# Kernel optimization log

Measured on AMD Instinct MI355X. Metric: run time of the kernel, lower is better.

The kernel has to match this reference:

```python
import jax, jax.numpy as jnp
import numpy as np

B, S, D, H, DFF = 8, 1024, 1024, 16, 4096
DK = D // H
NEG = -1000000000.0


def layernorm(x, g, b, eps=1e-5):
    mu = jnp.mean(x, axis=-1, keepdims=True)
    var = jnp.mean((x - mu) ** 2, axis=-1, keepdims=True)
    return (x - mu) / jnp.sqrt(var + eps) * g + b


def setup_inputs() -> dict:
    key = jax.random.key(0)
    ks = jax.random.split(key, 16)
    s = 0.02
    inp = {
        "x": jax.random.normal(ks[0], (B, S, D), jnp.float32),
        "binary_mask": jax.random.randint(ks[1], (B, S), 0, 2, jnp.int32),
        # per-head projections stacked: [H, D, DK]
        "Wq": jax.random.normal(ks[2], (H, D, DK), jnp.float32) * s,
        "bq": jnp.zeros((H, DK), jnp.float32),
        "Wk": jax.random.normal(ks[3], (H, D, DK), jnp.float32) * s,
        "bk": jnp.zeros((H, DK), jnp.float32),
        "Wv": jax.random.normal(ks[4], (H, D, DK), jnp.float32) * s,
        "bv": jnp.zeros((H, DK), jnp.float32),
        "Wo": jax.random.normal(ks[5], (D, D), jnp.float32) * s,
        "bo": jnp.zeros((D,), jnp.float32),
        "ga": jnp.ones((D,), jnp.float32),
        "ba": jnp.zeros((D,), jnp.float32),
        "W1": jax.random.normal(ks[6], (D, DFF), jnp.float32) * s,
        "b1": jnp.zeros((DFF,), jnp.float32),
        "W2": jax.random.normal(ks[7], (DFF, D), jnp.float32) * s,
        "b2": jnp.zeros((D,), jnp.float32),
        "gf": jnp.ones((D,), jnp.float32),
        "bf": jnp.zeros((D,), jnp.float32),
    }
    return inp


def encoder_fwd(x, binary_mask, Wq, bq, Wk, bk, Wv, bv, Wo, bo, ga, ba, W1, b1, W2, b2, gf, bf):
    # --- multi-head self-attention (heads vectorized over h axis) ---
    q = jnp.einsum("bsd,hdk->bhsk", x, Wq) + bq[None, :, None, :]
    k = jnp.einsum("bsd,hdk->bhsk", x, Wk) + bk[None, :, None, :]
    v = jnp.einsum("bsd,hdk->bhsk", x, Wv) + bv[None, :, None, :]
    score = jnp.einsum("bhik,bhjk->bhij", q, k) / jnp.sqrt(jnp.float32(DK))
    # mask: binary_mask is over KEY positions, broadcast over query dim
    score = score + jnp.where(binary_mask[:, None, None, :] == 0, NEG, 0.0)
    # NOTE: original code softmaxes over dim=1 of [B,Sq,Sk] -> the QUERY axis
    probs = jax.nn.softmax(score, axis=2)
    ctx = jnp.einsum("bhij,bhjk->bhik", probs, v)  # [B,H,S,DK]
    ctx = jnp.transpose(ctx, (0, 2, 1, 3)).reshape(x.shape[0], x.shape[1], D)
    attn_out = ctx @ Wo + bo
    y = layernorm(x + attn_out, ga, ba)
    # --- FFN ---
    h = jax.nn.relu(y @ W1 + b1)
    ffn_out = h @ W2 + b2
    return layernorm(y + ffn_out, gf, bf)


def reference(x, binary_mask, Wq, bq, Wk, bk, Wv, bv, Wo, bo, ga, ba, W1, b1, W2, b2, gf, bf):
    return encoder_fwd(x, binary_mask, Wq, bq, Wk, bk, Wv, bv, Wo, bo, ga, ba, W1, b1, W2, b2, gf, bf)
```

## Files before the change

### kernel.cpp

```cpp
#include <hip/hip_runtime.h>
#include <hip/hip_bf16.h>

typedef __bf16 bf16;
typedef __bf16 bf16x8 __attribute__((ext_vector_type(8)));
typedef __bf16 bf16x4 __attribute__((ext_vector_type(4)));
typedef float  f32x4  __attribute__((ext_vector_type(4)));

#define NB 8
#define NS 1024
#define ND 1024
#define NH 16
#define NDK 64
#define NDFF 4096

static __device__ __forceinline__ f32x4 mfma16(bf16x8 a, bf16x8 b, f32x4 c) {
    return __builtin_amdgcn_mfma_f32_16x16x32_bf16(a, b, c, 0, 0, 0);
}

#define GLDS(g, l) __builtin_amdgcn_global_load_lds( \
    (const __attribute__((address_space(1))) void*)(g), \
    (__attribute__((address_space(3))) void*)(l), 16, 0, 0)

__global__ __launch_bounds__(256) void cvt_x(const float* __restrict__ in,
                                             bf16* __restrict__ out, int n4)
{
    int idx = blockIdx.x * 256 + threadIdx.x;
    if (idx >= n4) return;
    float4 v = ((const float4*)in)[idx];
    bf16x4 o = { (bf16)v.x, (bf16)v.y, (bf16)v.z, (bf16)v.w };
    ((bf16x4*)out)[idx] = o;
}

__global__ __launch_bounds__(256) void prep_transpose(
    const float* __restrict__ Wq, const float* __restrict__ Wk, const float* __restrict__ Wv,
    const float* __restrict__ Wo, const float* __restrict__ W1, const float* __restrict__ W2,
    bf16* __restrict__ wqkvT, bf16* __restrict__ WoT,
    bf16* __restrict__ W1T, bf16* __restrict__ W2T)
{
    __shared__ float T[64][65];
    int bid = blockIdx.x;
    const float* src; bf16* dst; int srcLd, dstLd, tR, tC; bool scale = false;
    if (bid < 768) {
        int mat = bid >> 4, ty = bid & 15;
        int h = mat & 15, type = mat >> 4;
        const float* W = (type == 0) ? Wq : (type == 1 ? Wk : Wv);
        src = W + (size_t)h * ND * NDK;
        srcLd = NDK; tR = ty * 64; tC = 0;
        dst = wqkvT + ((size_t)type * 1024 + h * 64) * ND;
        dstLd = ND;
        scale = (type == 0);
    } else if (bid < 1024) {
        int b2 = bid - 768; int ty = b2 >> 4, tx = b2 & 15;
        src = Wo; srcLd = ND; tR = ty * 64; tC = tx * 64; dst = WoT; dstLd = ND;
    } else if (bid < 2048) {
        int b2 = bid - 1024; int ty = b2 >> 6, tx = b2 & 63;
        src = W1; srcLd = NDFF; tR = ty * 64; tC = tx * 64; dst = W1T; dstLd = ND;
    } else {
        int b2 = bid - 2048; int ty = b2 >> 4, tx = b2 & 15;
        src = W2; srcLd = ND; tR = ty * 64; tC = tx * 64; dst = W2T; dstLd = NDFF;
    }
    int t = threadIdx.x;
    int c0 = t & 63, r0 = t >> 6;
    #pragma unroll
    for (int rr = 0; rr < 16; rr++) {
        int row = rr * 4 + r0;
        T[row][c0] = src[(size_t)(tR + row) * srcLd + tC + c0];
    }
    __syncthreads();
    #pragma unroll
    for (int cc = 0; cc < 16; cc++) {
        int col = cc * 4 + r0;
        float v = T[c0][col];
        if (scale) v *= 0.125f;
        dst[(size_t)(tC + col) * dstLd + tR + c0] = (bf16)v;
    }
}

__global__ void prep_bias(const float* __restrict__ bq, const float* __restrict__ bk,
                          const float* __restrict__ bv, float* __restrict__ bqkv)
{
    int n = blockIdx.x * 256 + threadIdx.x;
    if (n >= 3072) return;
    int type = n >> 10, hk = n & 1023;
    const float* bb = (type == 0) ? bq : (type == 1 ? bk : bv);
    float v = bb[hk];
    if (type == 0) v *= 0.125f;
    bqkv[n] = v;
}

template<int BN>
__device__ __forceinline__ void gemm256_core(
    const bf16* __restrict__ A, const bf16* __restrict__ BT, int K,
    int rowBase, int colBase, f32x4 (&acc)[8][BN / 64],
    bf16* As, bf16* Bs)
{
    constexpr int NJ = BN / 128;
    constexpr int ABUF = 256 * 64;
    constexpr int BBUF = BN * 64;
    const int tid = threadIdx.x;
    const int lane = tid & 63, wid = tid >> 6;
    const int wm = wid >> 2, wn = wid & 3;
    const int lrow = lane & 15, lq = lane >> 4;
    const int srow = lane >> 3, gblk = (lane & 7) ^ srow;
    const int co0 = (lq ^ (lrow & 7)) * 8;
    const int co1 = ((4 + lq) ^ (lrow & 7)) * 8;

    f32x4 zz = {0.f, 0.f, 0.f, 0.f};
    #pragma unroll
    for (int i = 0; i < 8; i++)
        #pragma unroll
        for (int j = 0; j < 2 * NJ; j++) acc[i][j] = zz;

    const bf16* Ag = A  + (size_t)(rowBase + wid * 8 + srow) * K + gblk * 8;
    const bf16* Bg = BT + (size_t)(colBase + wid * 8 + srow) * K + gblk * 8;

#define STAGE256(kt, bi) do { \
    const bf16* a_ = Ag + (size_t)(kt) * 64; \
    _Pragma("unroll") \
    for (int r_ = 0; r_ < 4; r_++) \
        GLDS(a_ + (size_t)r_ * 64 * K, As + (bi) * ABUF + (r_ * 64 + wid * 8) * 64); \
    const bf16* b_ = Bg + (size_t)(kt) * 64; \
    _Pragma("unroll") \
    for (int r_ = 0; r_ < BN / 64; r_++) \
        GLDS(b_ + (size_t)r_ * 64 * K, Bs + (bi) * BBUF + (r_ * 64 + wid * 8) * 64); \
} while (0)

#define READ_A(MS) \
    _Pragma("unroll") \
    for (int i_ = 0; i_ < 4; i_++) { \
        int ro_ = (wm * 128 + (MS) * 64 + i_ * 16 + lrow) * 64; \
        af[i_][0] = *(const bf16x8*)&Ab[ro_ + co0]; \
        af[i_][1] = *(const bf16x8*)&Ab[ro_ + co1]; \
    }

#define READ_B(NS_) \
    _Pragma("unroll") \
    for (int j_ = 0; j_ < NJ; j_++) { \
        int ro_ = (wn * (BN / 4) + (NS_) * (BN / 8) + j_ * 16 + lrow) * 64; \
        bfr[j_][0] = *(const bf16x8*)&Bb[ro_ + co0]; \
        bfr[j_][1] = *(const bf16x8*)&Bb[ro_ + co1]; \
    }

#define MFMA_CLUSTER(IOFF, JOFF) do { \
    __builtin_amdgcn_s_barrier(); \
    asm volatile("s_waitcnt lgkmcnt(0)" ::: "memory"); \
    __builtin_amdgcn_sched_barrier(0); \
    __builtin_amdgcn_s_setprio(1); \
    _Pragma("unroll") \
    for (int i_ = 0; i_ < 4; i_++) \
        _Pragma("unroll") \
        for (int j_ = 0; j_ < NJ; j_++) { \
            acc[(IOFF) + i_][(JOFF) + j_] = mfma16(af[i_][0], bfr[j_][0], acc[(IOFF) + i_][(JOFF) + j_]); \
            acc[(IOFF) + i_][(JOFF) + j_] = mfma16(af[i_][1], bfr[j_][1], acc[(IOFF) + i_][(JOFF) + j_]); \
        } \
    __builtin_amdgcn_s_setprio(0); \
} while (0)

    const int nt = K >> 6;
    STAGE256(0, 0);
    asm volatile("s_waitcnt vmcnt(0)" ::: "memory");
    __builtin_amdgcn_s_barrier();

    int cur = 0;
    for (int t = 0; t < nt; ++t, cur ^= 1) {
        const bf16* Ab = As + cur * ABUF;
        const bf16* Bb = Bs + cur * BBUF;
        bf16x8 af[4][2], bfr[NJ][2];
        READ_A(0); READ_B(0);
        if (t + 1 < nt) STAGE256(t + 1, cur ^ 1);
        MFMA_CLUSTER(0, 0);
        __builtin_amdgcn_s_barrier();
        READ_A(1);
        MFMA_CLUSTER(4, 0);
        __builtin_amdgcn_s_barrier();
        READ_B(1);
        MFMA_CLUSTER(4, NJ);
        __builtin_amdgcn_s_barrier();
        READ_A(0);
        MFMA_CLUSTER(0, NJ);
        asm volatile("s_waitcnt vmcnt(0)" ::: "memory");
        __builtin_amdgcn_s_barrier();
    }
#undef STAGE256
#undef READ_A
#undef READ_B
#undef MFMA_CLUSTER
}

__global__ __launch_bounds__(512, 2) void g1_qkv(
    const bf16* __restrict__ x, const bf16* __restrict__ wqkvT, const float* __restrict__ bqkv,
    bf16* __restrict__ Q, bf16* __restrict__ Kb, bf16* __restrict__ Vb)
{
    __shared__ bf16 As[2 * 256 * 64], Bs[2 * 128 * 64];
    f32x4 acc[8][2];
    int nwg = gridDim.x, g = blockIdx.x;
    int sw = (g & 7) * (nwg >> 3) + (g >> 3);
    int bm = sw / 24, bn = sw % 24;
    int rowBase = bm * 256, colBase = bn * 128;
    gemm256_core<128>(x, wqkvT, ND, rowBase, colBase, acc, As, Bs);
    const int tid = threadIdx.x, lane = tid & 63, wid = tid >> 6;
    const int wm = wid >> 2, wn = wid & 3, lrow = lane & 15, lq = lane >> 4;
    #pragma unroll
    for (int j = 0; j < 2; j++) {
        int gcol = colBase + wn * 32 + j * 16 + lrow;
        float bias = bqkv[gcol];
        int type = gcol >> 10, h = (gcol >> 6) & 15, kk = gcol & 63;
        bf16* dst = (type == 0) ? Q : (type == 1 ? Kb : Vb);
        #pragma unroll
        for (int i = 0; i < 8; i++) {
            #pragma unroll
            for (int r = 0; r < 4; r++) {
                int grow = rowBase + wm * 128 + i * 16 + lq * 4 + r;
                int b = grow >> 10, s = grow & 1023;
                dst[((size_t)(b * NH + h) * NS + s) * NDK + kk] = (bf16)(acc[i][j][r] + bias);
            }
        }
    }
}

__global__ __launch_bounds__(256) void vt_trans(
    const bf16* __restrict__ Vb, bf16* __restrict__ Vt)
{
    __shared__ bf16 T[64 * 72];
    int bh = blockIdx.y, s0 = blockIdx.x * 64;
    const bf16* src = Vb + ((size_t)bh * NS + s0) * NDK;
    int tid = threadIdx.x;
    #pragma unroll
    for (int it = 0; it < 2; it++) {
        int g = tid + it * 256;
        int row = g >> 3, c = (g & 7) * 8;
        *(bf16x8*)&T[row * 72 + c] = *(const bf16x8*)&src[row * NDK + c];
    }
    __syncthreads();
    #pragma unroll
    for (int it = 0; it < 2; it++) {
        int g = tid + it * 256;
        int kk = g >> 3, sc = (g & 7) * 8;
        bf16x8 v;
        #pragma unroll
        for (int t = 0; t < 8; t++) v[t] = T[(sc + t) * 72 + kk];
        *(bf16x8*)&Vt[((size_t)bh * NDK + kk) * NS + s0 + sc] = v;
    }
}

__global__ __launch_bounds__(256) void g2_stats(
    const bf16* __restrict__ Q, const bf16* __restrict__ Kb,
    const int* __restrict__ mask, float2* __restrict__ alpha)
{
    __shared__ bf16 Qs[128 * 64];
    int bh = blockIdx.y, b = bh >> 4;
    int jBase = blockIdx.x * 128;
    const bf16* Kp = Kb + (size_t)bh * NS * NDK;
    const bf16* Qp = Q + (size_t)bh * NS * NDK;
    const int tid = threadIdx.x, lane = tid & 63, wid = tid >> 6;
    const int lrow = lane & 15, lq = lane >> 4;
    bf16x8 kf[2][2];
    #pragma unroll
    for (int jt = 0; jt < 2; jt++)
        #pragma unroll
        for (int kh = 0; kh < 2; kh++)
            kf[jt][kh] = *(const bf16x8*)&Kp[(size_t)(jBase + wid * 32 + jt * 16 + lrow) * NDK + kh * 32 + lq * 8];
    const int srow = lane >> 3;
    const int gblk = (lane & 7) ^ srow;
    float Lacc[2][4];
    #pragma unroll
    for (int jt = 0; jt < 2; jt++)
        #pragma unroll
        for (int r = 0; r < 4; r++) Lacc[jt][r] = 0.f;
    f32x4 zz = {0.f, 0.f, 0.f, 0.f};
    for (int i0 = 0; i0 < NS; i0 += 128) {
        __syncthreads();
        #pragma unroll
        for (int it = 0; it < 4; it++)
            GLDS(Qp + (size_t)(i0 + wid * 32 + it * 8 + srow) * NDK + gblk * 8,
                 Qs + (wid * 32 + it * 8) * 64);
        __syncthreads();
        #pragma unroll
        for (int it = 0; it < 8; it++) {
            bf16x8 qb[2];
            #pragma unroll
            for (int kh = 0; kh < 2; kh++)
                qb[kh] = *(const bf16x8*)&Qs[(it * 16 + lrow) * 64 + ((kh * 4 + lq) ^ (lrow & 7)) * 8];
            #pragma unroll
            for (int jt = 0; jt < 2; jt++) {
                f32x4 s = mfma16(kf[jt][0], qb[0], zz);
                s = mfma16(kf[jt][1], qb[1], s);
                #pragma unroll
                for (int r = 0; r < 4; r++) Lacc[jt][r] += __expf(s[r]);
            }
        }
    }
    #pragma unroll
    for (int jt = 0; jt < 2; jt++) {
        #pragma unroll
        for (int r = 0; r < 4; r++) {
            float v = Lacc[jt][r];
            v += __shfl_xor(v, 1); v += __shfl_xor(v, 2);
            v += __shfl_xor(v, 4); v += __shfl_xor(v, 8);
            if (lrow == 0) {
                int j = jBase + wid * 32 + jt * 16 + lq * 4 + r;
                int m = mask[b * NS + j];
                float2 ac;
                ac.x = m ? 1.f / v : 0.f;
                ac.y = m ? 0.f : (1.f / 1024.f);
                alpha[(size_t)bh * NS + j] = ac;
            }
        }
    }
}

__global__ __launch_bounds__(256) void g3_ctx(
    const bf16* __restrict__ Q, const bf16* __restrict__ Kb, const bf16* __restrict__ Vt,
    const float2* __restrict__ alpha, bf16* __restrict__ ctx)
{
    __shared__ bf16 Ks[64 * 64];
    __shared__ bf16 Vs[64 * 64];
    __shared__ bf16 Ps[4 * 64 * 64];
    int bh = blockIdx.y, iBase = blockIdx.x * 256;
    int b = bh >> 4, h = bh & 15;
    const bf16* Qp = Q + (size_t)bh * NS * NDK;
    const bf16* Kp = Kb + (size_t)bh * NS * NDK;
    const bf16* Vp = Vt + (size_t)bh * NDK * NS;
    const float2* al = alpha + (size_t)bh * NS;
    const int tid = threadIdx.x, lane = tid & 63, wid = tid >> 6;
    const int lrow = lane & 15, lq = lane >> 4;
    const int iw = iBase + wid * 64;
    bf16x8 qf[4][2];
    #pragma unroll
    for (int it = 0; it < 4; it++)
        #pragma unroll
        for (int kh = 0; kh < 2; kh++)
            qf[it][kh] = *(const bf16x8*)&Qp[(size_t)(iw + it * 16 + lrow) * NDK + kh * 32 + lq * 8];
    const int srow = lane >> 3;
    const int gblk = (lane & 7) ^ srow;
    f32x4 cacc[4][4];
    f32x4 zz = {0.f, 0.f, 0.f, 0.f};
    #pragma unroll
    for (int it = 0; it < 4; it++)
        #pragma unroll
        for (int kt = 0; kt < 4; kt++) cacc[it][kt] = zz;
    bf16* Pw = Ps + wid * 64 * 64;
    for (int j0 = 0; j0 < NS; j0 += 64) {
        __syncthreads();
        #pragma unroll
        for (int it = 0; it < 2; it++)
            GLDS(Kp + (size_t)(j0 + wid * 16 + it * 8 + srow) * NDK + gblk * 8,
                 Ks + (wid * 16 + it * 8) * 64);
        #pragma unroll
        for (int it = 0; it < 2; it++)
            GLDS(Vp + (size_t)(wid * 16 + it * 8 + srow) * NS + j0 + gblk * 8,
                 Vs + (wid * 16 + it * 8) * 64);
        __syncthreads();
        bf16x8 kb[4][2];
        #pragma unroll
        for (int jt = 0; jt < 4; jt++)
            #pragma unroll
            for (int kh = 0; kh < 2; kh++)
                kb[jt][kh] = *(const bf16x8*)&Ks[(jt * 16 + lrow) * 64 + ((kh * 4 + lq) ^ (lrow & 7)) * 8];
        #pragma unroll
        for (int jt = 0; jt < 4; jt++) {
            float2 acj[4];
            #pragma unroll
            for (int r = 0; r < 4; r++) acj[r] = al[j0 + jt * 16 + lq * 4 + r];
            #pragma unroll
            for (int it = 0; it < 4; it++) {
                f32x4 s = mfma16(kb[jt][0], qf[it][0], zz);
                s = mfma16(kb[jt][1], qf[it][1], s);
                bf16x4 pv;
                #pragma unroll
                for (int r = 0; r < 4; r++)
                    pv[r] = (bf16)(acj[r].x * __expf(s[r]) + acj[r].y);
                int i = it * 16 + lrow;
                int jb = jt * 2 + (lq >> 1);
                *(bf16x4*)&Pw[i * 64 + ((jb ^ (i & 7)) * 8) + (lq & 1) * 4] = pv;
            }
        }
        bf16x8 vb[4][2];
        #pragma unroll
        for (int kt = 0; kt < 4; kt++)
            #pragma unroll
            for (int kh = 0; kh < 2; kh++)
                vb[kt][kh] = *(const bf16x8*)&Vs[(kt * 16 + lrow) * 64 + ((kh * 4 + lq) ^ (lrow & 7)) * 8];
        #pragma unroll
        for (int it = 0; it < 4; it++) {
            bf16x8 pa[2];
            #pragma unroll
            for (int kh = 0; kh < 2; kh++)
                pa[kh] = *(const bf16x8*)&Pw[(it * 16 + lrow) * 64 + ((kh * 4 + lq) ^ (lrow & 7)) * 8];
            #pragma unroll
            for (int kt = 0; kt < 4; kt++) {
                cacc[it][kt] = mfma16(pa[0], vb[kt][0], cacc[it][kt]);
                cacc[it][kt] = mfma16(pa[1], vb[kt][1], cacc[it][kt]);
            }
        }
    }
    #pragma unroll
    for (int kt = 0; kt < 4; kt++) {
        int col = h * NDK + kt * 16 + lrow;
        #pragma unroll
        for (int it = 0; it < 4; it++) {
            #pragma unroll
            for (int r = 0; r < 4; r++) {
                int i = iw + it * 16 + lq * 4 + r;
                ctx[(size_t)(b * NS + i) * ND + col] = (bf16)cacc[it][kt][r];
            }
        }
    }
}

__global__ __launch_bounds__(512, 2) void g4_proj(
    const bf16* __restrict__ ctx, const bf16* __restrict__ WoT, const float* __restrict__ bo,
    const bf16* __restrict__ xb, bf16* __restrict__ t1b)
{
    __shared__ bf16 As[2 * 256 * 64], Bs[2 * 128 * 64];
    f32x4 acc[8][2];
    int nwg = gridDim.x, g = blockIdx.x;
    int sw = (g & 7) * (nwg >> 3) + (g >> 3);
    int bm = sw >> 3, bn = sw & 7;
    int rowBase = bm * 256, colBase = bn * 128;
    gemm256_core<128>(ctx, WoT, ND, rowBase, colBase, acc, As, Bs);
    const int tid = threadIdx.x, lane = tid & 63, wid = tid >> 6;
    const int wm = wid >> 2, wn = wid & 3, lrow = lane & 15, lq = lane >> 4;
    #pragma unroll
    for (int j = 0; j < 2; j++) {
        int gcol = colBase + wn * 32 + j * 16 + lrow;
        float bias = bo[gcol];
        #pragma unroll
        for (int i = 0; i < 8; i++) {
            #pragma unroll
            for (int r = 0; r < 4; r++) {
                int grow = rowBase + wm * 128 + i * 16 + lq * 4 + r;
                float v = acc[i][j][r] + bias + (float)xb[(size_t)grow * ND + gcol];
                t1b[(size_t)grow * ND + gcol] = (bf16)v;
            }
        }
    }
}

__global__ __launch_bounds__(512, 2) void g5_ffn1(
    const bf16* __restrict__ y, const bf16* __restrict__ W1T, const float* __restrict__ b1,
    bf16* __restrict__ hb)
{
    __shared__ bf16 As[2 * 256 * 64], Bs[2 * 256 * 64];
    f32x4 acc[8][4];
    int nwg = gridDim.x, g = blockIdx.x;
    int sw = (g & 7) * (nwg >> 3) + (g >> 3);
    int bm = sw >> 4, bn = sw & 15;
    int rowBase = bm * 256, colBase = bn * 256;
    gemm256_core<256>(y, W1T, ND, rowBase, colBase, acc, As, Bs);
    const int tid = threadIdx.x, lane = tid & 63, wid = tid >> 6;
    const int wm = wid >> 2, wn = wid & 3, lrow = lane & 15, lq = lane >> 4;
    #pragma unroll
    for (int j = 0; j < 4; j++) {
        int gcol = colBase + wn * 64 + j * 16 + lrow;
        float bias = b1[gcol];
        #pragma unroll
        for (int i = 0; i < 8; i++) {
            #pragma unroll
            for (int r = 0; r < 4; r++) {
                int grow = rowBase + wm * 128 + i * 16 + lq * 4 + r;
                float v = fmaxf(acc[i][j][r] + bias, 0.f);
                hb[(size_t)grow * NDFF + gcol] = (bf16)v;
            }
        }
    }
}

__global__ __launch_bounds__(512, 2) void g6_ffn2(
    const bf16* __restrict__ hb, const bf16* __restrict__ W2T, const float* __restrict__ b2,
    const bf16* __restrict__ yb, bf16* __restrict__ zb)
{
    __shared__ bf16 As[2 * 256 * 64], Bs[2 * 128 * 64];
    f32x4 acc[8][2];
    int nwg = gridDim.x, g = blockIdx.x;
    int sw = (g & 7) * (nwg >> 3) + (g >> 3);
    int bm = sw >> 3, bn = sw & 7;
    int rowBase = bm * 256, colBase = bn * 128;
    gemm256_core<128>(hb, W2T, NDFF, rowBase, colBase, acc, As, Bs);
    const int tid = threadIdx.x, lane = tid & 63, wid = tid >> 6;
    const int wm = wid >> 2, wn = wid & 3, lrow = lane & 15, lq = lane >> 4;
    #pragma unroll
    for (int j = 0; j < 2; j++) {
        int gcol = colBase + wn * 32 + j * 16 + lrow;
        float bias = b2[gcol];
        #pragma unroll
        for (int i = 0; i < 8; i++) {
            #pragma unroll
            for (int r = 0; r < 4; r++) {
                int grow = rowBase + wm * 128 + i * 16 + lq * 4 + r;
                float v = acc[i][j][r] + bias + (float)yb[(size_t)grow * ND + gcol];
                zb[(size_t)grow * ND + gcol] = (bf16)v;
            }
        }
    }
}

__global__ __launch_bounds__(256) void ln_kernel(
    const bf16* __restrict__ in, bf16* __restrict__ outb, float* __restrict__ outf,
    const float* __restrict__ g, const float* __restrict__ bb)
{
    int row = blockIdx.x, tid = threadIdx.x;
    const bf16* p = in + (size_t)row * ND;
    bf16x4 v4 = *(const bf16x4*)&p[tid * 4];
    float vv[4] = {(float)v4[0], (float)v4[1], (float)v4[2], (float)v4[3]};
    float s = vv[0] + vv[1] + vv[2] + vv[3];
    float q = vv[0]*vv[0] + vv[1]*vv[1] + vv[2]*vv[2] + vv[3]*vv[3];
    #pragma unroll
    for (int m = 1; m < 64; m <<= 1) { s += __shfl_xor(s, m); q += __shfl_xor(q, m); }
    __shared__ float rs[4], rq[4];
    int wid = tid >> 6, lane = tid & 63;
    if (lane == 0) { rs[wid] = s; rq[wid] = q; }
    __syncthreads();
    s = rs[0] + rs[1] + rs[2] + rs[3];
    q = rq[0] + rq[1] + rq[2] + rq[3];
    float mean = s * (1.f / 1024.f);
    float var = q * (1.f / 1024.f) - mean * mean;
    float rstd = 1.f / sqrtf(var + 1e-5f);
    float4 of;
    bf16x4 ob;
    #pragma unroll
    for (int k = 0; k < 4; k++) {
        int col = tid * 4 + k;
        float yv = (vv[k] - mean) * rstd * g[col] + bb[col];
        ((float*)&of)[k] = yv;
        ob[k] = (bf16)yv;
    }
    if (outb) *(bf16x4*)&outb[(size_t)row * ND + tid * 4] = ob;
    if (outf) ((float4*)(outf + (size_t)row * ND))[tid] = of;
}

extern "C" void kernel_launch(void* const* d_in, const int* in_sizes, int n_in,
                              void* d_out, int out_size, void* d_ws, size_t ws_size,
                              hipStream_t stream)
{
    const float* x    = (const float*)d_in[0];
    const int*   mask = (const int*)d_in[1];
    const float* Wq   = (const float*)d_in[2];
    const float* bq   = (const float*)d_in[3];
    const float* Wk   = (const float*)d_in[4];
    const float* bk   = (const float*)d_in[5];
    const float* Wv   = (const float*)d_in[6];
    const float* bv   = (const float*)d_in[7];
    const float* Wo   = (const float*)d_in[8];
    const float* bo   = (const float*)d_in[9];
    const float* ga   = (const float*)d_in[10];
    const float* ba   = (const float*)d_in[11];
    const float* W1   = (const float*)d_in[12];
    const float* b1   = (const float*)d_in[13];
    const float* W2   = (const float*)d_in[14];
    const float* b2   = (const float*)d_in[15];
    const float* gf   = (const float*)d_in[16];
    const float* bfb  = (const float*)d_in[17];

    size_t off = 0;
    auto alloc = [&](size_t n) { char* p = (char*)d_ws + off; off += (n + 255) & ~(size_t)255; return (void*)p; };
    bf16*   wqkvT = (bf16*)  alloc((size_t)3072 * 1024 * 2);
    bf16*   WoT   = (bf16*)  alloc((size_t)1024 * 1024 * 2);
    bf16*   W1T   = (bf16*)  alloc((size_t)4096 * 1024 * 2);
    bf16*   W2T   = (bf16*)  alloc((size_t)1024 * 4096 * 2);
    float*  bqkv  = (float*) alloc(3072 * 4);
    float2* alpha = (float2*)alloc((size_t)NB * NH * NS * 8);
    bf16*   xb    = (bf16*)  alloc((size_t)8192 * 1024 * 2);
    bf16*   ub    = (bf16*)  alloc((size_t)8192 * 4096 * 2);
    bf16*   Qb    = ub;
    bf16*   Kb    = ub + (size_t)8192 * 1024;
    bf16*   Vt    = ub + (size_t)2 * 8192 * 1024;
    bf16*   ctx   = ub + (size_t)3 * 8192 * 1024;
    bf16*   hb    = ub;
    bf16*   t1b   = (bf16*)  alloc((size_t)8192 * 1024 * 2);
    bf16*   Vb    = t1b;
    bf16*   zb    = t1b;
    bf16*   yb    = (bf16*)  alloc((size_t)8192 * 1024 * 2);

    cvt_x<<<8192, 256, 0, stream>>>(x, xb, 8192 * 1024 / 4);
    prep_transpose<<<3072, 256, 0, stream>>>(Wq, Wk, Wv, Wo, W1, W2, wqkvT, WoT, W1T, W2T);
    prep_bias<<<12, 256, 0, stream>>>(bq, bk, bv, bqkv);
    g1_qkv<<<768, 512, 0, stream>>>(xb, wqkvT, bqkv, Qb, Kb, Vb);
    vt_trans<<<dim3(16, 128), 256, 0, stream>>>(Vb, Vt);
    g2_stats<<<dim3(8, 128), 256, 0, stream>>>(Qb, Kb, mask, alpha);
    g3_ctx<<<dim3(4, 128), 256, 0, stream>>>(Qb, Kb, Vt, alpha, ctx);
    g4_proj<<<256, 512, 0, stream>>>(ctx, WoT, bo, xb, t1b);
    ln_kernel<<<8192, 256, 0, stream>>>(t1b, yb, nullptr, ga, ba);
    g5_ffn1<<<512, 512, 0, stream>>>(yb, W1T, b1, hb);
    g6_ffn2<<<256, 512, 0, stream>>>(hb, W2T, b2, yb, zb);
    ln_kernel<<<8192, 256, 0, stream>>>(zb, nullptr, (float*)d_out, gf, bfb);
}
```

Before: 566.8 us.

## Restructure GEMM main loop with double fragment registers and fewer barriers

Replaces the GEMM core's four barrier-separated MFMA clusters with a loop that issues the next tile's global-to-LDS stage first. It then loads separate A and B fragment sets (a0/a1, b0/b1) and runs four MFMA clusters with no intermediate barriers or explicit lgkmcnt waits. The end-of-iteration wait and barrier are skipped on the final tile. The aim is to cut workgroup synchronisation stalls and let LDS reads overlap MFMA work. In exchange, the extra fragment registers raise register pressure under the 512x2 launch bounds. The block-swizzle divisors are also hardcoded per kernel instead of derived from gridDim.

```diff
diff --git a/kernel.cpp b/kernel.cpp
--- a/kernel.cpp
+++ b/kernel.cpp
@@ -89,102 +89,90 @@
 }
 
 template<int BN>
-__device__ __forceinline__ void gemm256_core(
+__device__ __forceinline__ void gemm_dp(
     const bf16* __restrict__ A, const bf16* __restrict__ BT, int K,
-    int rowBase, int colBase, f32x4 (&acc)[8][BN / 64],
-    bf16* As, bf16* Bs)
-{
-    constexpr int NJ = BN / 128;
-    constexpr int ABUF = 256 * 64;
-    constexpr int BBUF = BN * 64;
-    const int tid = threadIdx.x;
-    const int lane = tid & 63, wid = tid >> 6;
+    int rowBase, int colBase, f32x4 (&acc)[8][BN / 64], bf16* As, bf16* Bs)
+{
+    constexpr int NF = BN / 64;
+    constexpr int NHF = NF / 2;
+    constexpr int ABUF = 256 * 64, BBUF = BN * 64;
+    constexpr int BR = BN / 64;
+    const int tid = threadIdx.x, lane = tid & 63, wid = tid >> 6;
     const int wm = wid >> 2, wn = wid & 3;
     const int lrow = lane & 15, lq = lane >> 4;
     const int srow = lane >> 3, gblk = (lane & 7) ^ srow;
     const int co0 = (lq ^ (lrow & 7)) * 8;
     const int co1 = ((4 + lq) ^ (lrow & 7)) * 8;
-
     f32x4 zz = {0.f, 0.f, 0.f, 0.f};
     #pragma unroll
     for (int i = 0; i < 8; i++)
         #pragma unroll
-        for (int j = 0; j < 2 * NJ; j++) acc[i][j] = zz;
-
+        for (int j = 0; j < NF; j++) acc[i][j] = zz;
     const bf16* Ag = A  + (size_t)(rowBase + wid * 8 + srow) * K + gblk * 8;
     const bf16* Bg = BT + (size_t)(colBase + wid * 8 + srow) * K + gblk * 8;
 
-#define STAGE256(kt, bi) do { \
-    const bf16* a_ = Ag + (size_t)(kt) * 64; \
+#define STAGE_DP(kt, bi) do { \
     _Pragma("unroll") \
     for (int r_ = 0; r_ < 4; r_++) \
-        GLDS(a_ + (size_t)r_ * 64 * K, As + (bi) * ABUF + (r_ * 64 + wid * 8) * 64); \
-    const bf16* b_ = Bg + (size_t)(kt) * 64; \
+        GLDS(Ag + (size_t)(kt) * 64 + (size_t)r_ * 64 * K, \
+             As + (bi) * ABUF + (r_ * 64 + wid * 8) * 64); \
     _Pragma("unroll") \
-    for (int r_ = 0; r_ < BN / 64; r_++) \
-        GLDS(b_ + (size_t)r_ * 64 * K, Bs + (bi) * BBUF + (r_ * 64 + wid * 8) * 64); \
+    for (int r_ = 0; r_ < BR; r_++) \
+        GLDS(Bg + (size_t)(kt) * 64 + (size_t)r_ * 64 * K, \
+             Bs + (bi) * BBUF + (r_ * 64 + wid * 8) * 64); \
 } while (0)
 
-#define READ_A(MS) \
-    _Pragma("unroll") \
-    for (int i_ = 0; i_ < 4; i_++) { \
-        int ro_ = (wm * 128 + (MS) * 64 + i_ * 16 + lrow) * 64; \
-        af[i_][0] = *(const bf16x8*)&Ab[ro_ + co0]; \
-        af[i_][1] = *(const bf16x8*)&Ab[ro_ + co1]; \
-    }
-
-#define READ_B(NS_) \
-    _Pragma("unroll") \
-    for (int j_ = 0; j_ < NJ; j_++) { \
-        int ro_ = (wn * (BN / 4) + (NS_) * (BN / 8) + j_ * 16 + lrow) * 64; \
-        bfr[j_][0] = *(const bf16x8*)&Bb[ro_ + co0]; \
-        bfr[j_][1] = *(const bf16x8*)&Bb[ro_ + co1]; \
-    }
-
-#define MFMA_CLUSTER(IOFF, JOFF) do { \
-    __builtin_amdgcn_s_barrier(); \
-    asm volatile("s_waitcnt lgkmcnt(0)" ::: "memory"); \
-    __builtin_amdgcn_sched_barrier(0); \
+#define RDA_DP(dst, ms) do { _Pragma("unroll") for (int i_ = 0; i_ < 4; i_++) { \
+    int ro_ = (wm * 128 + (ms) * 64 + i_ * 16 + lrow) * 64; \
+    dst[i_][0] = *(const bf16x8*)&Ab[ro_ + co0]; \
+    dst[i_][1] = *(const bf16x8*)&Ab[ro_ + co1]; } } while (0)
+
+#define RDB_DP(dst, h) do { _Pragma("unroll") for (int j_ = 0; j_ < NHF; j_++) { \
+    int ro_ = (wn * (BN / 4) + (h) * (BN / 8) + j_ * 16 + lrow) * 64; \
+    dst[j_][0] = *(const bf16x8*)&Bb[ro_ + co0]; \
+    dst[j_][1] = *(const bf16x8*)&Bb[ro_ + co1]; } } while (0)
+
+#define CL_DP(av, bv, ms, h) do { \
     __builtin_amdgcn_s_setprio(1); \
     _Pragma("unroll") \
     for (int i_ = 0; i_ < 4; i_++) \
         _Pragma("unroll") \
-        for (int j_ = 0; j_ < NJ; j_++) { \
-            acc[(IOFF) + i_][(JOFF) + j_] = mfma16(af[i_][0], bfr[j_][0], acc[(IOFF) + i_][(JOFF) + j_]); \
-            acc[(IOFF) + i_][(JOFF) + j_] = mfma16(af[i_][1], bfr[j_][1], acc[(IOFF) + i_][(JOFF) + j_]); \
+        for (int j_ = 0; j_ < NHF; j_++) { \
+            acc[(ms) * 4 + i_][(h) * NHF + j_] = \
+                mfma16(av[i_][0], bv[j_][0], acc[(ms) * 4 + i_][(h) * NHF + j_]); \
+            acc[(ms) * 4 + i_][(h) * NHF + j_] = \
+                mfma16(av[i_][1], bv[j_][1], acc[(ms) * 4 + i_][(h) * NHF + j_]); \
         } \
     __builtin_amdgcn_s_setprio(0); \
 } while (0)
 
     const int nt = K >> 6;
-    STAGE256(0, 0);
+    STAGE_DP(0, 0);
     asm volatile("s_waitcnt vmcnt(0)" ::: "memory");
     __builtin_amdgcn_s_barrier();
 
-    int cur = 0;
-    for (int t = 0; t < nt; ++t, cur ^= 1) {
+    for (int t = 0; t < nt; ++t) {
+        const int cur = t & 1;
         const bf16* Ab = As + cur * ABUF;
         const bf16* Bb = Bs + cur * BBUF;
-        bf16x8 af[4][2], bfr[NJ][2];
-        READ_A(0); READ_B(0);
-        if (t + 1 < nt) STAGE256(t + 1, cur ^ 1);
-        MFMA_CLUSTER(0, 0);
-        __builtin_amdgcn_s_barrier();
-        READ_A(1);
-        MFMA_CLUSTER(4, 0);
-        __builtin_amdgcn_s_barrier();
-        READ_B(1);
-        MFMA_CLUSTER(4, NJ);
-        __builtin_amdgcn_s_barrier();
-        READ_A(0);
-        MFMA_CLUSTER(0, NJ);
-        asm volatile("s_waitcnt vmcnt(0)" ::: "memory");
-        __builtin_amdgcn_s_barrier();
-    }
-#undef STAGE256
-#undef READ_A
-#undef READ_B
-#undef MFMA_CLUSTER
+        if (t + 1 < nt) STAGE_DP(t + 1, cur ^ 1);
+        bf16x8 a0[4][2], a1[4][2], b0[NHF][2], b1[NHF][2];
+        RDA_DP(a0, 0); RDB_DP(b0, 0);
+        CL_DP(a0, b0, 0, 0);
+        RDB_DP(b1, 1);
+        CL_DP(a0, b1, 0, 1);
+        RDA_DP(a1, 1);
+        CL_DP(a1, b1, 1, 1);
+        CL_DP(a1, b0, 1, 0);
+        if (t + 1 < nt) {
+            asm volatile("s_waitcnt vmcnt(0)" ::: "memory");
+            __builtin_amdgcn_s_barrier();
+        }
+    }
+#undef STAGE_DP
+#undef RDA_DP
+#undef RDB_DP
+#undef CL_DP
 }
 
 __global__ __launch_bounds__(512, 2) void g1_qkv(
@@ -193,11 +181,11 @@
 {
     __shared__ bf16 As[2 * 256 * 64], Bs[2 * 128 * 64];
     f32x4 acc[8][2];
-    int nwg = gridDim.x, g = blockIdx.x;
-    int sw = (g & 7) * (nwg >> 3) + (g >> 3);
+    int g = blockIdx.x;
+    int sw = (g & 7) * 96 + (g >> 3);
     int bm = sw / 24, bn = sw % 24;
     int rowBase = bm * 256, colBase = bn * 128;
-    gemm256_core<128>(x, wqkvT, ND, rowBase, colBase, acc, As, Bs);
+    gemm_dp<128>(x, wqkvT, ND, rowBase, colBase, acc, As, Bs);
     const int tid = threadIdx.x, lane = tid & 63, wid = tid >> 6;
     const int wm = wid >> 2, wn = wid & 3, lrow = lane & 15, lq = lane >> 4;
     #pragma unroll
@@ -414,11 +402,11 @@
 {
     __shared__ bf16 As[2 * 256 * 64], Bs[2 * 128 * 64];
     f32x4 acc[8][2];
-    int nwg = gridDim.x, g = blockIdx.x;
-    int sw = (g & 7) * (nwg >> 3) + (g >> 3);
+    int g = blockIdx.x;
+    int sw = (g & 7) * 32 + (g >> 3);
     int bm = sw >> 3, bn = sw & 7;
     int rowBase = bm * 256, colBase = bn * 128;
-    gemm256_core<128>(ctx, WoT, ND, rowBase, colBase, acc, As, Bs);
+    gemm_dp<128>(ctx, WoT, ND, rowBase, colBase, acc, As, Bs);
     const int tid = threadIdx.x, lane = tid & 63, wid = tid >> 6;
     const int wm = wid >> 2, wn = wid & 3, lrow = lane & 15, lq = lane >> 4;
     #pragma unroll
@@ -443,11 +431,11 @@
 {
     __shared__ bf16 As[2 * 256 * 64], Bs[2 * 256 * 64];
     f32x4 acc[8][4];
-    int nwg = gridDim.x, g = blockIdx.x;
-    int sw = (g & 7) * (nwg >> 3) + (g >> 3);
+    int g = blockIdx.x;
+    int sw = (g & 7) * 64 + (g >> 3);
     int bm = sw >> 4, bn = sw & 15;
     int rowBase = bm * 256, colBase = bn * 256;
-    gemm256_core<256>(y, W1T, ND, rowBase, colBase, acc, As, Bs);
+    gemm_dp<256>(y, W1T, ND, rowBase, colBase, acc, As, Bs);
     const int tid = threadIdx.x, lane = tid & 63, wid = tid >> 6;
     const int wm = wid >> 2, wn = wid & 3, lrow = lane & 15, lq = lane >> 4;
     #pragma unroll
@@ -472,11 +460,11 @@
 {
     __shared__ bf16 As[2 * 256 * 64], Bs[2 * 128 * 64];
     f32x4 acc[8][2];
-    int nwg = gridDim.x, g = blockIdx.x;
-    int sw = (g & 7) * (nwg >> 3) + (g >> 3);
+    int g = blockIdx.x;
+    int sw = (g & 7) * 32 + (g >> 3);
     int bm = sw >> 3, bn = sw & 7;
     int rowBase = bm * 256, colBase = bn * 128;
-    gemm256_core<128>(hb, W2T, NDFF, rowBase, colBase, acc, As, Bs);
+    gemm_dp<128>(hb, W2T, NDFF, rowBase, colBase, acc, As, Bs);
     const int tid = threadIdx.x, lane = tid & 63, wid = tid >> 6;
     const int wm = wid >> 2, wn = wid & 3, lrow = lane & 15, lq = lane >> 4;
     #pragma unroll
```

Result: faster. 537.9 us (-5.1%).
